# Kernel tuning notes

Measured on AMD Instinct MI355X. Metric: run time of the kernel, lower is better.

## Reference

```python
import jax, jax.numpy as jnp
import numpy as np
from jax import lax

N = 100000
IN_C, HID, OUT_C = 512, 256, 128
K_STEPS = 10
ALPHA = 0.1
RES_ALPHA = 1.0
LN_EPS = 1e-5


def layer_norm(h, g, b):
    mu = jnp.mean(h, axis=-1, keepdims=True)
    var = jnp.mean(jnp.square(h - mu), axis=-1, keepdims=True)
    return (h - mu) * lax.rsqrt(var + LN_EPS) * g + b


def appnp(h, src, dst):
    # add self loops
    loop = jnp.arange(N, dtype=src.dtype)
    s = jnp.concatenate([src, loop])
    d = jnp.concatenate([dst, loop])
    ew = jnp.ones(s.shape[0], h.dtype)
    deg = jax.ops.segment_sum(ew, d, num_segments=N)
    dis = jnp.where(deg > 0, lax.rsqrt(jnp.maximum(deg, 1e-12)), 0.0)
    norm = dis[s] * ew * dis[d]  # [E+N]
    h0 = h
    def step(carry, _):
        msg = norm[:, None] * carry[s]                      # gather [E+N, C]
        agg = jax.ops.segment_sum(msg, d, num_segments=N)    # scatter-add
        return (1.0 - ALPHA) * agg + ALPHA * h0, None
    h, _ = lax.scan(step, h, None, length=K_STEPS)
    return h


def setup_inputs() -> dict:
    key = jax.random.key(0)
    ks = jax.random.split(key, 12)
    def lin(k, fan_in, fan_out):
        bound = 1.0 / np.sqrt(fan_in)
        kw, kb = jax.random.split(k)
        W = jax.random.uniform(kw, (fan_in, fan_out), jnp.float32, -bound, bound)
        b = jax.random.uniform(kb, (fan_out,), jnp.float32, -bound, bound)
        return W, b
    x = jax.random.normal(ks[0], (N, IN_C), jnp.float32)
    edge_index = jax.random.randint(ks[1], (2, 1600000), 0, N, jnp.int32)
    W_in, b_in = lin(ks[2], IN_C, HID)
    W1, b1 = lin(ks[3], HID, HID)
    W2, b2 = lin(ks[4], HID, HID)
    W_out, b_out = lin(ks[5], HID, OUT_C)
    g1 = jnp.ones(HID); be1 = jnp.zeros(HID)
    g2 = jnp.ones(HID); be2 = jnp.zeros(HID)
    return {"x": x, "edge_index": edge_index,
            "W_in": W_in, "b_in": b_in,
            "W1": W1, "b1": b1, "g1": g1, "be1": be1,
            "W2": W2, "b2": b2, "g2": g2, "be2": be2,
            "W_out": W_out, "b_out": b_out}


def reference(x, edge_index, W_in, b_in, W1, b1, g1, be1, W2, b2, g2, be2, W_out, b_out):
    # MLP with residual blocks (eval mode: no dropout)
    h = x @ W_in + b_in
    for (W, b, g, be) in ((W1, b1, g1, be1), (W2, b2, g2, be2)):
        identity = h
        h = layer_norm(h @ W + b, g, be)
        h = RES_ALPHA * h + (1.0 - RES_ALPHA) * identity
        h = jax.nn.relu(h)
    h = h @ W_out + b_out
    # APPNP propagation
    return appnp(h, edge_index[0], edge_index[1])
```

## Files before the change

kernel.cpp:

```cpp
#include <hip/hip_runtime.h>

typedef unsigned short u16;
typedef unsigned long long u64;
typedef __attribute__((ext_vector_type(8))) short bfrag;
typedef __attribute__((ext_vector_type(4))) float f32x4;

__device__ inline float b2f(u16 u) {
    union { unsigned int i; float f; } v; v.i = ((unsigned int)u) << 16; return v.f;
}
__device__ inline u16 f2b(float f) {
    union { float f; unsigned int u; } v; v.f = f;
    unsigned int r = v.u + 0x7fffu + ((v.u >> 16) & 1u);
    return (u16)(r >> 16);
}
__device__ inline float ldF(const void* p, size_t i, bool bf) {
    return bf ? b2f(((const u16*)p)[i]) : ((const float*)p)[i];
}
__device__ inline void gload_lds16(const void* g, void* l) {
    __builtin_amdgcn_global_load_lds((const __attribute__((address_space(1))) unsigned int*)g,
                                     (__attribute__((address_space(3))) unsigned int*)l, 16, 0, 0);
}

__global__ void detect_k(const unsigned int* __restrict__ g1w, int* flag) {
    if (blockIdx.x == 0 && threadIdx.x == 0)
        *flag = (g1w[0] == 0x3F803F80u) ? 1 : 0;
}

__global__ void wt_k(const void* __restrict__ W, u16* __restrict__ Wt, int K, int NC,
                     const int* __restrict__ flagp) {
    int i = blockIdx.x * 256 + threadIdx.x;
    if (i >= K * NC) return;
    int k = i / NC, nn = i - k * NC;
    u16 v = (*flagp) ? ((const u16*)W)[i] : f2b(((const float*)W)[i]);
    Wt[(size_t)nn * K + k] = v;
}

template<int K, bool A_DUAL>
__global__ __launch_bounds__(256) void gemm_bt(const void* __restrict__ Ain, const u16* __restrict__ Bt,
                                               const void* __restrict__ bias, u16* __restrict__ C,
                                               int M, int NC, const int* __restrict__ flagp) {
    const int BM = 128, BN = 128, BK = 32;
    __shared__ u16 sh[16384];
    const bool bf = (*flagp != 0);
    int nt = NC / BN;

    int nwg = gridDim.x, bid = blockIdx.x;
    int qc = nwg >> 3, rc = nwg & 7;
    int xcd = bid & 7, off = bid >> 3;
    int swz = (xcd < rc ? xcd * (qc + 1) : rc * (qc + 1) + (xcd - rc) * qc) + off;
    int m0 = (swz / nt) * BM;
    int n0 = (swz % nt) * BN;

    int t = threadIdx.x;
    int lane = t & 63, wave = t >> 6;
    int wm = (wave >> 1) * 64, wn = (wave & 1) * 64;

    f32x4 acc[4][4];
#pragma unroll
    for (int i = 0; i < 4; i++)
#pragma unroll
        for (int j = 0; j < 4; j++) acc[i][j] = (f32x4){0.f, 0.f, 0.f, 0.f};

    char* shb = (char*)sh;
    auto ldsA = [&](int bufi) { return shb + bufi * 8192; };
    auto ldsB = [&](int bufi) { return shb + 16384 + bufi * 8192; };

    auto stageAsync = [&](int bufi, int kk) {
#pragma unroll
        for (int q = 0; q < 2; ++q) {
            int idx = q * 256 + t, row = idx >> 2, cb = (idx & 3) * 16;
            int ra = m0 + row; ra = ra < M ? ra : M - 1;
            gload_lds16((const char*)Bt + ((size_t)(n0 + row) * K + kk) * 2 + cb,
                        ldsB(bufi) + q * 4096 + wave * 1024);
            if (!A_DUAL || bf)
                gload_lds16((const char*)Ain + ((size_t)ra * K + kk) * 2 + cb,
                            ldsA(bufi) + q * 4096 + wave * 1024);
        }
    };
    float4 fr[2][2];
    auto loadA32 = [&](int kk) {
#pragma unroll
        for (int q = 0; q < 2; ++q) {
            int idx = q * 256 + t, row = idx >> 2, cf = (idx & 3) * 8;
            int ra = m0 + row; ra = ra < M ? ra : M - 1;
            const float* g = (const float*)Ain + (size_t)ra * K + kk + cf;
            fr[q][0] = *(const float4*)g;
            fr[q][1] = *(const float4*)(g + 4);
        }
    };
    auto writeA32 = [&](int bufi) {
#pragma unroll
        for (int q = 0; q < 2; ++q) {
            ushort4 o0, o1;
            o0.x = f2b(fr[q][0].x); o0.y = f2b(fr[q][0].y); o0.z = f2b(fr[q][0].z); o0.w = f2b(fr[q][0].w);
            o1.x = f2b(fr[q][1].x); o1.y = f2b(fr[q][1].y); o1.z = f2b(fr[q][1].z); o1.w = f2b(fr[q][1].w);
            char* la = ldsA(bufi) + q * 4096 + wave * 1024 + lane * 16;
            *(ushort4*)la = o0;
            *(ushort4*)(la + 8) = o1;
        }
    };

    const bool a32 = A_DUAL && !bf;
    if (a32) loadA32(0);
    stageAsync(0, 0);
    if (a32) writeA32(0);
    __syncthreads();
    int cur = 0;
    int r16 = lane & 15, q8 = (lane >> 4) * 8;
    for (int k0 = 0; k0 < K; k0 += BK) {
        bool next = (k0 + BK < K);
        if (next) {
            if (a32) loadA32(k0 + BK);
            stageAsync(cur ^ 1, k0 + BK);
        }
        const u16* Ac = (const u16*)ldsA(cur);
        const u16* Bc = (const u16*)ldsB(cur);
        bfrag a[4], b[4];
#pragma unroll
        for (int i = 0; i < 4; i++) a[i] = *(const bfrag*)&Ac[(wm + i * 16 + r16) * BK + q8];
#pragma unroll
        for (int j = 0; j < 4; j++) b[j] = *(const bfrag*)&Bc[(wn + j * 16 + r16) * BK + q8];
#pragma unroll
        for (int i = 0; i < 4; i++)
#pragma unroll
            for (int j = 0; j < 4; j++)
                acc[i][j] = __builtin_amdgcn_mfma_f32_16x16x32_bf16(a[i], b[j], acc[i][j], 0, 0, 0);
        if (next && a32) writeA32(cur ^ 1);
        __syncthreads();
        cur ^= 1;
    }

    int q4 = (lane >> 4) * 4;
#pragma unroll
    for (int j = 0; j < 4; j++) {
        int cg = n0 + wn + j * 16 + r16;
        float bvv = ldF(bias, cg, bf);
        int colb = (wn + j * 16 + r16) * 2;
#pragma unroll
        for (int i = 0; i < 4; i++) {
#pragma unroll
            for (int rr = 0; rr < 4; rr++) {
                int row = wm + i * 16 + q4 + rr;
                int sw = colb ^ (((row >> 2) & 3) << 5);
                *(u16*)(shb + row * 256 + sw) = f2b(acc[i][j][rr] + bvv);
            }
        }
    }
    __syncthreads();
#pragma unroll
    for (int pass = 0; pass < 8; ++pass) {
        int u = pass * 256 + t;
        int row = u >> 4;
        int cb = (u & 15) * 16;
        int sw = cb ^ (((row >> 2) & 3) << 5);
        uint4 vv = *(const uint4*)(shb + row * 256 + sw);
        int rg = m0 + row;
        if (rg < M)
            *(uint4*)((char*)C + ((size_t)rg * NC + n0) * 2 + cb) = vv;
    }
}

__global__ __launch_bounds__(256) void ln_relu_k(const u16* __restrict__ T, const void* __restrict__ g,
                                                 const void* __restrict__ be, u16* __restrict__ out,
                                                 int M, const int* __restrict__ flagp) {
    const bool bf = (*flagp != 0);
    int wave = threadIdx.x >> 6, lane = threadIdx.x & 63;
    int row = blockIdx.x * 4 + wave;
    if (row >= M) return;
    const ushort4 xq = *(const ushort4*)(T + (size_t)row * 256 + lane * 4);
    float x0 = b2f(xq.x), x1 = b2f(xq.y), x2 = b2f(xq.z), x3 = b2f(xq.w);
    float s = x0 + x1 + x2 + x3;
    for (int o = 32; o > 0; o >>= 1) s += __shfl_xor(s, o);
    float mu = s * (1.0f / 256.0f);
    float d0 = x0 - mu, d1 = x1 - mu, d2 = x2 - mu, d3 = x3 - mu;
    float q = d0 * d0 + d1 * d1 + d2 * d2 + d3 * d3;
    for (int o = 32; o > 0; o >>= 1) q += __shfl_xor(q, o);
    float rs = rsqrtf(q * (1.0f / 256.0f) + 1e-5f);
    int c0 = lane * 4;
    float y0 = fmaxf(d0 * rs * ldF(g, c0 + 0, bf) + ldF(be, c0 + 0, bf), 0.f);
    float y1 = fmaxf(d1 * rs * ldF(g, c0 + 1, bf) + ldF(be, c0 + 1, bf), 0.f);
    float y2 = fmaxf(d2 * rs * ldF(g, c0 + 2, bf) + ldF(be, c0 + 2, bf), 0.f);
    float y3 = fmaxf(d3 * rs * ldF(g, c0 + 3, bf) + ldF(be, c0 + 3, bf), 0.f);
    ushort4 o4; o4.x = f2b(y0); o4.y = f2b(y1); o4.z = f2b(y2); o4.w = f2b(y3);
    *(ushort4*)(out + (size_t)row * 256 + c0) = o4;
}

__global__ void deg_count(const int* __restrict__ dst, int* deg, int E) {
    int i = blockIdx.x * 256 + threadIdx.x;
    if (i < E) atomicAdd(&deg[dst[i]], 1);
}
__global__ void dis_k(const int* __restrict__ deg, float* dis, int n) {
    int i = blockIdx.x * 256 + threadIdx.x;
    if (i < n) dis[i] = rsqrtf((float)(deg[i] + 1));
}

__global__ void scan_block(const int* __restrict__ deg, int* rowptr, int* bsum, int n) {
    __shared__ int sh[256];
    int t = threadIdx.x, i = blockIdx.x * 256 + t;
    int v = (i < n) ? deg[i] + 1 : 0;
    sh[t] = v; __syncthreads();
    for (int o = 1; o < 256; o <<= 1) {
        int x = (t >= o) ? sh[t - o] : 0;
        __syncthreads();
        sh[t] += x;
        __syncthreads();
    }
    if (i < n) rowptr[i] = sh[t] - v;
    if (t == 255) bsum[blockIdx.x] = sh[t];
}
__global__ void scan_sums(int* bsum, int nb) {
    __shared__ int sh[512];
    int t = threadIdx.x;
    int v = (t < nb) ? bsum[t] : 0;
    sh[t] = v; __syncthreads();
    for (int o = 1; o < 512; o <<= 1) {
        int x = (t >= o) ? sh[t - o] : 0;
        __syncthreads();
        sh[t] += x;
        __syncthreads();
    }
    if (t < nb) bsum[t] = sh[t] - v;
}
__global__ void scan_add(int* rowptr, const int* __restrict__ bsum, int n, int total) {
    int i = blockIdx.x * 256 + threadIdx.x;
    if (i < n) rowptr[i] += bsum[blockIdx.x];
    if (i == 0) rowptr[n] = total;
}
__global__ void fill_k(const int* __restrict__ src, const int* __restrict__ dst,
                       const int* __restrict__ rowptr, int* cursor, const float* __restrict__ dis,
                       int2* __restrict__ epack, int E, int n) {
    int i = blockIdx.x * 256 + threadIdx.x;
    if (i >= E + n) return;
    int s, d;
    if (i < E) { s = src[i]; d = dst[i]; }
    else       { s = d = i - E; }
    int p = rowptr[d] + atomicAdd(&cursor[d], 1);
    float wv = dis[s] * dis[d];
    u64 e = ((u64)__float_as_uint(wv) << 32) | (unsigned int)s;
    __builtin_nontemporal_store(e, (u64*)&epack[p]);
}

__global__ __launch_bounds__(256) void prop_k(const u16* __restrict__ curb, const u16* __restrict__ h0b,
                                              const int* __restrict__ rowptr, const int2* __restrict__ epack,
                                              u16* __restrict__ outB, void* __restrict__ outD,
                                              const int* __restrict__ flagp, int n) {
    int wave = threadIdx.x >> 6, lane = threadIdx.x & 63;
    int node = blockIdx.x * 4 + wave;
    if (node >= n) return;
    int p0 = rowptr[node], p1 = rowptr[node + 1];
    float ax = 0.f, ay = 0.f;
    for (int p = p0; p < p1; p += 64) {
        int cnt = p1 - p; if (cnt > 64) cnt = 64;
        int sj = 0; float wj = 0.f;
        if (lane < cnt) {
            u64 e = __builtin_nontemporal_load((const u64*)(epack + p + lane));
            sj = (int)(unsigned int)e;
            wj = __uint_as_float((unsigned int)(e >> 32));
        }
        int j = 0;
        for (; j + 16 <= cnt; j += 16) {
            float ww[16]; unsigned int v[16];
#pragma unroll
            for (int u = 0; u < 16; ++u) {
                int ss = __shfl(sj, j + u);
                ww[u] = __shfl(wj, j + u);
                v[u] = *(const unsigned int*)(curb + (size_t)ss * 128 + 2 * lane);
            }
#pragma unroll
            for (int u = 0; u < 16; ++u) {
                ax = fmaf(ww[u], b2f((u16)(v[u] & 0xffffu)), ax);
                ay = fmaf(ww[u], b2f((u16)(v[u] >> 16)), ay);
            }
        }
        for (; j < cnt; j += 8) {
            float ww[8]; unsigned int v[8];
#pragma unroll
            for (int u = 0; u < 8; ++u) {
                int jj = j + u;
                bool ok = jj < cnt;
                if (!ok) jj = cnt - 1;
                int ss = __shfl(sj, jj);
                float w2 = __shfl(wj, jj);
                ww[u] = ok ? w2 : 0.f;
                v[u] = *(const unsigned int*)(curb + (size_t)ss * 128 + 2 * lane);
            }
#pragma unroll
            for (int u = 0; u < 8; ++u) {
                ax = fmaf(ww[u], b2f((u16)(v[u] & 0xffffu)), ax);
                ay = fmaf(ww[u], b2f((u16)(v[u] >> 16)), ay);
            }
        }
    }
    unsigned int hp = __builtin_nontemporal_load((const unsigned int*)h0b + (size_t)node * 64 + lane);
    float rx = 0.9f * ax + 0.1f * b2f((u16)(hp & 0xffffu));
    float ry = 0.9f * ay + 0.1f * b2f((u16)(hp >> 16));
    unsigned int pk = ((unsigned int)f2b(ry) << 16) | (unsigned int)f2b(rx);
    if (outB) {
        __builtin_nontemporal_store(pk, (unsigned int*)outB + (size_t)node * 64 + lane);
    } else if (*flagp) {
        __builtin_nontemporal_store(pk, (unsigned int*)outD + (size_t)node * 64 + lane);
    } else {
        u64 o = ((u64)__float_as_uint(ry) << 32) | __float_as_uint(rx);
        __builtin_nontemporal_store(o, (u64*)((float*)outD + (size_t)node * 128 + 2 * lane));
    }
}

extern "C" void kernel_launch(void* const* d_in, const int* in_sizes, int n_in,
                              void* d_out, int out_size, void* d_ws, size_t ws_size,
                              hipStream_t stream) {
    const int N = in_sizes[0] / 512;
    const int E = in_sizes[1] / 2;
    const void* x    = d_in[0];
    const int*  ei   = (const int*)d_in[1];
    const void* Win  = d_in[2];
    const void* bin  = d_in[3];
    const void* W1   = d_in[4];
    const void* b1   = d_in[5];
    const void* g1   = d_in[6];
    const void* be1  = d_in[7];
    const void* W2   = d_in[8];
    const void* b2   = d_in[9];
    const void* g2   = d_in[10];
    const void* be2  = d_in[11];
    const void* Wout = d_in[12];
    const void* bout = d_in[13];
    (void)n_in; (void)out_size; (void)ws_size;

    char* w = (char*)d_ws;
    auto alloc = [&](size_t b) { char* p = w; w += (b + 255) & ~(size_t)255; return p; };
    char*  buf0 = alloc((size_t)N * 512 * 2);
    char*  actAraw = alloc((size_t)N * 256 * 2);
    u16* WtIn  = (u16*)alloc((size_t)512 * 256 * 2);
    u16* Wt1   = (u16*)alloc((size_t)256 * 256 * 2);
    u16* Wt2   = (u16*)alloc((size_t)256 * 256 * 2);
    u16* WtOut = (u16*)alloc((size_t)256 * 128 * 2);
    int*   deg    = (int*)alloc((size_t)N * 4);
    float* dis    = (float*)alloc((size_t)N * 4);
    int*   rowptr = (int*)alloc((size_t)(N + 1) * 4);
    int*   cursor = (int*)alloc((size_t)N * 4);
    int*   bsum   = (int*)alloc(512 * 4);
    int*   flag   = (int*)alloc(256);
    u16*   Tb  = (u16*)buf0;
    u16*   h0b = (u16*)buf0;
    u16*   cA  = (u16*)(buf0 + (size_t)N * 128 * 2);
    u16*   cB  = (u16*)(buf0 + (size_t)N * 128 * 4);
    u16*   actA  = (u16*)actAraw;
    int2*  epack = (int2*)actAraw;

    detect_k<<<1, 64, 0, stream>>>((const unsigned int*)g1, flag);

    wt_k<<<(512 * 256 + 255) / 256, 256, 0, stream>>>(Win,  WtIn,  512, 256, flag);
    wt_k<<<(256 * 256 + 255) / 256, 256, 0, stream>>>(W1,   Wt1,   256, 256, flag);
    wt_k<<<(256 * 256 + 255) / 256, 256, 0, stream>>>(W2,   Wt2,   256, 256, flag);
    wt_k<<<(256 * 128 + 255) / 256, 256, 0, stream>>>(Wout, WtOut, 256, 128, flag);

    int mt = (N + 127) / 128;
    gemm_bt<512, true ><<<mt * 2, 256, 0, stream>>>(x,    WtIn,  bin,  actA, N, 256, flag);
    gemm_bt<256, false><<<mt * 2, 256, 0, stream>>>(actA, Wt1,   b1,   Tb,   N, 256, flag);
    ln_relu_k<<<(N + 3) / 4, 256, 0, stream>>>(Tb, g1, be1, actA, N, flag);
    gemm_bt<256, false><<<mt * 2, 256, 0, stream>>>(actA, Wt2,   b2,   Tb,   N, 256, flag);
    ln_relu_k<<<(N + 3) / 4, 256, 0, stream>>>(Tb, g2, be2, actA, N, flag);
    gemm_bt<256, false><<<mt * 1, 256, 0, stream>>>(actA, WtOut, bout, h0b,  N, 128, flag);

    hipMemsetAsync(deg, 0, (size_t)N * 4, stream);
    deg_count<<<(E + 255) / 256, 256, 0, stream>>>(ei + E, deg, E);
    dis_k    <<<(N + 255) / 256, 256, 0, stream>>>(deg, dis, N);
    int nb = (N + 255) / 256;
    scan_block<<<nb, 256, 0, stream>>>(deg, rowptr, bsum, N);
    scan_sums<<<1, 512, 0, stream>>>(bsum, nb);
    scan_add<<<nb, 256, 0, stream>>>(rowptr, bsum, N, E + N);
    hipMemsetAsync(cursor, 0, (size_t)N * 4, stream);
    fill_k<<<(E + N + 255) / 256, 256, 0, stream>>>(ei, ei + E, rowptr, cursor, dis, epack, E, N);

    const u16* cur = h0b;
    for (int it = 0; it < 10; ++it) {
        bool last = (it == 9);
        u16* o = (it & 1) ? cB : cA;
        prop_k<<<(N + 3) / 4, 256, 0, stream>>>(cur, h0b, rowptr, epack,
                                                last ? nullptr : o,
                                                last ? d_out : nullptr, flag, N);
        cur = o;
    }
}
```

Before: 1.370 ms.

## Deepen GEMM bf16 path to a 4-stage LDS ring with prefetch distance two

When A is already bf16, the GEMM now uses a four-buffer LDS ring instead of double buffering. It issues async global-to-LDS loads two K-steps ahead, uses explicit s_waitcnt vmcnt counts, and needs a single s_barrier per iteration. The fp32-A path keeps the old double-buffered loop but only stages B asynchronously. The aim is to hide global load latency for the MLP GEMMs. In exchange, shared memory grows to 64KB per block, which can lower occupancy, and the code relies on hand-counted vmcnt values being correct.

Result: no change. 1.366 ms (-0.3%).

```diff
diff --git a/kernel.cpp b/kernel.cpp
--- a/kernel.cpp
+++ b/kernel.cpp
@@ -40,7 +40,8 @@
                                                const void* __restrict__ bias, u16* __restrict__ C,
                                                int M, int NC, const int* __restrict__ flagp) {
     const int BM = 128, BN = 128, BK = 32;
-    __shared__ u16 sh[16384];
+    const int KI = K / BK;
+    __shared__ u16 sh[32768];
     const bool bf = (*flagp != 0);
     int nt = NC / BN;
 
@@ -63,7 +64,7 @@
 
     char* shb = (char*)sh;
     auto ldsA = [&](int bufi) { return shb + bufi * 8192; };
-    auto ldsB = [&](int bufi) { return shb + 16384 + bufi * 8192; };
+    auto ldsB = [&](int bufi) { return shb + 32768 + bufi * 8192; };
 
     auto stageAsync = [&](int bufi, int kk) {
 #pragma unroll
@@ -72,9 +73,16 @@
             int ra = m0 + row; ra = ra < M ? ra : M - 1;
             gload_lds16((const char*)Bt + ((size_t)(n0 + row) * K + kk) * 2 + cb,
                         ldsB(bufi) + q * 4096 + wave * 1024);
-            if (!A_DUAL || bf)
-                gload_lds16((const char*)Ain + ((size_t)ra * K + kk) * 2 + cb,
-                            ldsA(bufi) + q * 4096 + wave * 1024);
+            gload_lds16((const char*)Ain + ((size_t)ra * K + kk) * 2 + cb,
+                        ldsA(bufi) + q * 4096 + wave * 1024);
+        }
+    };
+    auto stageB = [&](int bufi, int kk) {
+#pragma unroll
+        for (int q = 0; q < 2; ++q) {
+            int idx = q * 256 + t, row = idx >> 2, cb = (idx & 3) * 16;
+            gload_lds16((const char*)Bt + ((size_t)(n0 + row) * K + kk) * 2 + cb,
+                        ldsB(bufi) + q * 4096 + wave * 1024);
         }
     };
     float4 fr[2][2];
@@ -100,35 +108,59 @@
         }
     };
 
+    int r16 = lane & 15, q8 = (lane >> 4) * 8;
     const bool a32 = A_DUAL && !bf;
-    if (a32) loadA32(0);
-    stageAsync(0, 0);
-    if (a32) writeA32(0);
+
+    if (!a32) {
+        stageAsync(0, 0);
+        stageAsync(1, BK);
+#pragma unroll
+        for (int ki = 0; ki < KI; ++ki) {
+            if (ki + 2 < KI) stageAsync((ki + 2) & 3, (ki + 2) * BK);
+            if (ki + 2 < KI)       asm volatile("s_waitcnt vmcnt(8)" ::: "memory");
+            else if (ki + 2 == KI) asm volatile("s_waitcnt vmcnt(4)" ::: "memory");
+            else                   asm volatile("s_waitcnt vmcnt(0)" ::: "memory");
+            asm volatile("s_barrier" ::: "memory");
+            const u16* Ac = (const u16*)ldsA(ki & 3);
+            const u16* Bc = (const u16*)ldsB(ki & 3);
+            bfrag a[4], b[4];
+#pragma unroll
+            for (int i = 0; i < 4; i++) a[i] = *(const bfrag*)&Ac[(wm + i * 16 + r16) * BK + q8];
+#pragma unroll
+            for (int j = 0; j < 4; j++) b[j] = *(const bfrag*)&Bc[(wn + j * 16 + r16) * BK + q8];
+#pragma unroll
+            for (int i = 0; i < 4; i++)
+#pragma unroll
+                for (int j = 0; j < 4; j++)
+                    acc[i][j] = __builtin_amdgcn_mfma_f32_16x16x32_bf16(a[i], b[j], acc[i][j], 0, 0, 0);
+        }
+    } else {
+        loadA32(0);
+        stageB(0, 0);
+        writeA32(0);
+        __syncthreads();
+        int cur = 0;
+        for (int k0 = 0; k0 < K; k0 += BK) {
+            bool next = (k0 + BK < K);
+            if (next) { loadA32(k0 + BK); stageB(cur ^ 1, k0 + BK); }
+            const u16* Ac = (const u16*)ldsA(cur);
+            const u16* Bc = (const u16*)ldsB(cur);
+            bfrag a[4], b[4];
+#pragma unroll
+            for (int i = 0; i < 4; i++) a[i] = *(const bfrag*)&Ac[(wm + i * 16 + r16) * BK + q8];
+#pragma unroll
+            for (int j = 0; j < 4; j++) b[j] = *(const bfrag*)&Bc[(wn + j * 16 + r16) * BK + q8];
+#pragma unroll
+            for (int i = 0; i < 4; i++)
+#pragma unroll
+                for (int j = 0; j < 4; j++)
+                    acc[i][j] = __builtin_amdgcn_mfma_f32_16x16x32_bf16(a[i], b[j], acc[i][j], 0, 0, 0);
+            if (next) writeA32(cur ^ 1);
+            __syncthreads();
+            cur ^= 1;
+        }
+    }
     __syncthreads();
-    int cur = 0;
-    int r16 = lane & 15, q8 = (lane >> 4) * 8;
-    for (int k0 = 0; k0 < K; k0 += BK) {
-        bool next = (k0 + BK < K);
-        if (next) {
-            if (a32) loadA32(k0 + BK);
-            stageAsync(cur ^ 1, k0 + BK);
-        }
-        const u16* Ac = (const u16*)ldsA(cur);
-        const u16* Bc = (const u16*)ldsB(cur);
-        bfrag a[4], b[4];
-#pragma unroll
-        for (int i = 0; i < 4; i++) a[i] = *(const bfrag*)&Ac[(wm + i * 16 + r16) * BK + q8];
-#pragma unroll
-        for (int j = 0; j < 4; j++) b[j] = *(const bfrag*)&Bc[(wn + j * 16 + r16) * BK + q8];
-#pragma unroll
-        for (int i = 0; i < 4; i++)
-#pragma unroll
-            for (int j = 0; j < 4; j++)
-                acc[i][j] = __builtin_amdgcn_mfma_f32_16x16x32_bf16(a[i], b[j], acc[i][j], 0, 0, 0);
-        if (next && a32) writeA32(cur ^ 1);
-        __syncthreads();
-        cur ^= 1;
-    }
 
     int q4 = (lane >> 4) * 4;
 #pragma unroll
```
